# Kernel tuning notes

Hardware: AMD Instinct MI355X
Metric: run time of the kernel (lower is better)

Reference implementation:

```python
import jax, jax.numpy as jnp
import numpy as np

HEADS = 2


def _log_cpb(h, w, w1, b1, w2):
    # Swin-v2 style continuous relative position bias on an h*w grid.
    yy, xx = jnp.meshgrid(jnp.arange(h), jnp.arange(w), indexing='ij')
    coords = jnp.stack([yy.reshape(-1), xx.reshape(-1)], axis=-1).astype(jnp.float32)  # (L, 2)
    rel = coords[:, None, :] - coords[None, :, :]                                      # (L, L, 2)
    denom = jnp.array([max(h - 1, 1), max(w - 1, 1)], dtype=jnp.float32)
    rel = rel / denom * 8.0
    rel = jnp.sign(rel) * jnp.log2(1.0 + jnp.abs(rel)) / np.float32(np.log2(8.0))
    bias = jax.nn.relu(rel @ w1.T + b1) @ w2.T                                         # (L, L, heads)
    return jnp.transpose(bias, (2, 0, 1))                                              # (heads, L, L)


def setup_inputs() -> dict:
    key = jax.random.key(0)
    ks = jax.random.split(key, 11)
    b, s, c, h, w = 2, 32, 128, 24, 24
    hid, out_ch = 256, 128
    sc = lambda n: 1.0 / np.sqrt(n)
    return {
        'x':      jax.random.normal(ks[0], (b, s, c, h, w), jnp.float32),
        'qk_w':   jax.random.normal(ks[1], (2 * c, c), jnp.float32) * sc(c),
        'v_w':    jax.random.normal(ks[2], (hid, c), jnp.float32) * sc(c),
        'cpb_w1': jax.random.normal(ks[3], (c, 2), jnp.float32) * sc(2),
        'cpb_b1': jax.random.normal(ks[4], (c,), jnp.float32) * 0.02,
        'cpb_w2': jax.random.normal(ks[5], (HEADS, c), jnp.float32) * sc(c),
        'sa_bias': jax.random.uniform(ks[6], (hid, 1, 1), jnp.float32, -sc(c), sc(c)),
        'mlp_w1': jax.random.normal(ks[7], (hid, hid), jnp.float32) * sc(hid),
        'mlp_b1': jax.random.normal(ks[8], (hid,), jnp.float32) * 0.02,
        'mlp_w2': jax.random.normal(ks[9], (out_ch, hid), jnp.float32) * sc(hid),
        'mlp_b2': jax.random.normal(ks[10], (out_ch,), jnp.float32) * 0.02,
    }


def reference(x, qk_w, v_w, cpb_w1, cpb_b1, cpb_w2, sa_bias, mlp_w1, mlp_b1, mlp_w2, mlp_b2):
    b, s, c, h, w = x.shape
    L = h * w
    qkd = c // HEADS
    vd = v_w.shape[0] // HEADS
    xr = x.reshape(b * s, c, L)                                        # flatten (b s) and (h w)
    # QKV via 1x1 convs == channel matmuls
    qk = jnp.einsum('oc,bcl->bol', qk_w, xr)                           # (bs, 2c, L)
    qk = qk.reshape(b * s, 2, HEADS, qkd, L).transpose(1, 0, 2, 4, 3)  # (2, bs, heads, L, d)
    q, k = qk[0], qk[1]
    v = jnp.einsum('oc,bcl->bol', v_w, xr).reshape(b * s, HEADS, vd, L).transpose(0, 1, 3, 2)
    # learned continuous relative position bias, added as SDPA attn_mask
    bias = _log_cpb(h, w, cpb_w1, cpb_b1, cpb_w2)                      # (heads, L, L)
    scale = np.float32(1.0 / np.sqrt(qkd))
    scores = jnp.einsum('bhld,bhmd->bhlm', q, k) * scale + bias[None]
    attn = jax.nn.softmax(scores, axis=-1)
    out = jnp.einsum('bhlm,bhmd->bhld', attn, v)                       # (bs, heads, L, vd)
    out = out.transpose(0, 1, 3, 2).reshape(b, s, HEADS * vd, h, w)
    out = out + sa_bias[None, None]                                    # (b, s, hid, h, w)
    # 1x1-conv MLP with exact GELU
    y = jnp.einsum('oi,bsihw->bsohw', mlp_w1, out) + mlp_b1[None, None, :, None, None]
    y = jax.nn.gelu(y, approximate=False)
    y = jnp.einsum('oi,bsihw->bsohw', mlp_w2, y) + mlp_b2[None, None, :, None, None]
    return y
```

## Files before the change

### kernel.cpp

```cpp
#include <hip/hip_runtime.h>
#include <cstdint>
#include <cstddef>

constexpr int BS   = 64;
constexpr int Cc   = 128;
constexpr int Lc   = 576;
constexpr int VD   = 128;
constexpr int HID  = 256;
constexpr int OUTC = 128;
constexpr int NPIX = BS * Lc;

typedef __bf16 bf16x8 __attribute__((ext_vector_type(8)));
typedef float  f32x4  __attribute__((ext_vector_type(4)));
typedef unsigned short u16x8 __attribute__((ext_vector_type(8)));
typedef unsigned int   u32x4 __attribute__((ext_vector_type(4)));

__device__ __forceinline__ unsigned short f2bf(float f) {
  unsigned int u = __builtin_bit_cast(unsigned int, f);
  u += 0x7fffu + ((u >> 16) & 1u);
  return (unsigned short)(u >> 16);
}
__device__ __forceinline__ float bf2f(unsigned short h) {
  unsigned int u = ((unsigned int)h) << 16;
  return __builtin_bit_cast(float, u);
}
__device__ __forceinline__ unsigned int packhl(float v) {
  unsigned short hi = f2bf(v);
  unsigned short lo = f2bf(v - bf2f(hi));
  return ((unsigned int)hi << 16) | (unsigned int)lo;
}
__device__ __forceinline__ void unpack8(u32x4 a, u32x4 b, bf16x8& hi, bf16x8& lo) {
  u32x4 h, l;
  h[0] = (a[1] & 0xffff0000u) | (a[0] >> 16);
  l[0] = (a[1] << 16)         | (a[0] & 0xffffu);
  h[1] = (a[3] & 0xffff0000u) | (a[2] >> 16);
  l[1] = (a[3] << 16)         | (a[2] & 0xffffu);
  h[2] = (b[1] & 0xffff0000u) | (b[0] >> 16);
  l[2] = (b[1] << 16)         | (b[0] & 0xffffu);
  h[3] = (b[3] & 0xffff0000u) | (b[2] >> 16);
  l[3] = (b[3] << 16)         | (b[2] & 0xffffu);
  hi = __builtin_bit_cast(bf16x8, h);
  lo = __builtin_bit_cast(bf16x8, l);
}

#define MFMA16(a, b, c) __builtin_amdgcn_mfma_f32_16x16x32_bf16((a), (b), (c), 0, 0, 0)

__global__ __launch_bounds__(256) void cpb_kernel(const float* __restrict__ w1,
                                                  const float* __restrict__ b1,
                                                  const float* __restrict__ w2,
                                                  float* __restrict__ tab) {
  int idx = blockIdx.x * 256 + threadIdx.x;
  if (idx >= 47 * 47) return;
  int dy = idx / 47 - 23, dx = idx % 47 - 23;
  float fy = (float)dy * (8.0f / 23.0f);
  float fx = (float)dx * (8.0f / 23.0f);
  fy = copysignf(log2f(1.0f + fabsf(fy)) * (1.0f / 3.0f), fy);
  fx = copysignf(log2f(1.0f + fabsf(fx)) * (1.0f / 3.0f), fx);
  float a0 = 0.f, a1 = 0.f;
  for (int hh = 0; hh < 128; hh++) {
    float hv = fmaxf(w1[2 * hh] * fy + w1[2 * hh + 1] * fx + b1[hh], 0.f);
    a0 += w2[hh] * hv;
    a1 += w2[128 + hh] * hv;
  }
  tab[idx] = a0;
  tab[2209 + idx] = a1;
}

__global__ __launch_bounds__(256) void bias_mat(const float* __restrict__ tab,
                                                unsigned short* __restrict__ biasC) {
  int id = blockIdx.x * 256 + threadIdx.x;
  if (id >= 737280) return;
  int id2 = id % 2560;
  int grp = id / 2560;
  int wave = grp & 3;
  int mt = (grp >> 2) % 36;
  int hh = grp / 144;
  int g = id2 / 512;
  int lane = (id2 >> 3) & 63;
  int k = id2 & 7;
  int e = g * 8 + k;
  unsigned short val = 0;
  if (e < 36) {
    int ln = e >> 2, r = e & 3;
    int nt = wave * 9 + ln;
    int i = mt * 16 + (lane >> 4) * 4 + r;
    int j = nt * 16 + (lane & 15);
    int yi = i / 24, xi = i - yi * 24;
    int yj = j / 24, xj = j - yj * 24;
    val = f2bf(tab[hh * 2209 + (yi - yj + 23) * 47 + (xi - xj + 23)]);
  }
  biasC[id] = val;
}

__global__ __launch_bounds__(256) void prep_w(
    const float* __restrict__ w1, const float* __restrict__ w2,
    const float* __restrict__ qkw, const float* __restrict__ vw,
    unsigned short* __restrict__ w1h, unsigned short* __restrict__ w1l,
    unsigned short* __restrict__ w2h, unsigned short* __restrict__ w2l,
    unsigned short* __restrict__ wqkh, unsigned short* __restrict__ wqkl,
    unsigned short* __restrict__ wvh, unsigned short* __restrict__ wvl) {
  int id = blockIdx.x * 256 + threadIdx.x;
  const float* src;
  unsigned short *dh, *dl;
  int off;
  if (id < 65536)       { src = w1;  dh = w1h;  dl = w1l;  off = id; }
  else if (id < 98304)  { src = w2;  dh = w2h;  dl = w2l;  off = id - 65536; }
  else if (id < 131072) { src = qkw; dh = wqkh; dl = wqkl; off = id - 98304; }
  else if (id < 163840) { src = vw;  dh = wvh;  dl = wvl;  off = id - 131072; }
  else return;
  float v = src[off];
  unsigned short hi = f2bf(v);
  dh[off] = hi;
  dl[off] = f2bf(v - bf2f(hi));
}

__global__ __launch_bounds__(256) void prep_x(const float* __restrict__ x,
                                              unsigned short* __restrict__ xph,
                                              unsigned short* __restrict__ xpl) {
  __shared__ float xt[128 * 65];
  const int l0 = blockIdx.x * 64, bs = blockIdx.y;
  const int t = threadIdx.x;
  const float* xb = x + (size_t)bs * Cc * Lc;
#pragma unroll
  for (int pass = 0; pass < 8; pass++) {
    int f = pass * 1024 + t * 4;
    int c = f >> 6, ll = f & 63;
    *(float4*)(xt + c * 65 + ll) = *(const float4*)(xb + c * Lc + l0 + ll);
  }
  __syncthreads();
  const int rowl = t >> 2, c0 = (t & 3) * 32;
  const size_t p = (size_t)bs * Lc + l0 + rowl;
  unsigned short hbuf[32], lbuf[32];
#pragma unroll
  for (int i = 0; i < 32; i++) {
    float v = xt[(c0 + i) * 65 + rowl];
    unsigned short hi = f2bf(v);
    hbuf[i] = hi;
    lbuf[i] = f2bf(v - bf2f(hi));
  }
#pragma unroll
  for (int g = 0; g < 4; g++) {
    *(u16x8*)(xph + p * 128 + c0 + g * 8) = *(u16x8*)(hbuf + g * 8);
    *(u16x8*)(xpl + p * 128 + c0 + g * 8) = *(u16x8*)(lbuf + g * 8);
  }
}

__global__ __launch_bounds__(256, 2) void qkv_mfma(
    const unsigned short* __restrict__ xh, const unsigned short* __restrict__ xl,
    const unsigned short* __restrict__ wqkh, const unsigned short* __restrict__ wqkl,
    const unsigned short* __restrict__ wvh, const unsigned short* __restrict__ wvl,
    unsigned short* __restrict__ qg, unsigned short* __restrict__ kg,
    unsigned short* __restrict__ vg) {
  __shared__ unsigned short vt[128 * 130];
  const int t = threadIdx.x;
  const int wv = t >> 6, lane = t & 63;
  const int quad = lane >> 4, cc = lane & 15;
  const int by = blockIdx.y;
  const int n0 = (wv >> 1) * 64;
  const unsigned short* Wh = (by < 2) ? wqkh : wvh;
  const unsigned short* Wl = (by < 2) ? wqkl : wvl;
  const int wrow0 = (by & 1) * 128 + n0;
  f32x4 acc[4][4];
#pragma unroll
  for (int i = 0; i < 4; i++)
#pragma unroll
    for (int j = 0; j < 4; j++) acc[i][j] = (f32x4){0.f, 0.f, 0.f, 0.f};
  {
    const int srow = lane >> 3;
    const int schunk = (lane & 7) ^ srow;
    const size_t grow = (size_t)(blockIdx.x * 128 + wv * 32 + srow) * 128;
    const unsigned short* asrc = (schunk < 4)
                                     ? (xh + grow + (schunk << 3))
                                     : (xl + grow + ((schunk - 4) << 3));
    unsigned short* adst = vt + wv * 2048;
#pragma unroll
    for (int s = 0; s < 4; s++)
      __builtin_amdgcn_global_load_lds(
          (const __attribute__((address_space(1))) unsigned int*)(asrc + s * 1024),
          (__attribute__((address_space(3))) unsigned int*)(adst + s * 512),
          16, 0, 0);
    for (int kc = 0; kc < 4; kc++) {
      __syncthreads();
      const int bufo = (kc & 1) << 13;
      bf16x8 Ah[4], Al[4], Bh[4], Bl[4];
#pragma unroll
      for (int i = 0; i < 4; i++) {
        const int row = (wv & 1) * 64 + i * 16 + cc;
        const unsigned short* ab = vt + bufo + row * 64;
        Ah[i] = *(const bf16x8*)(ab + ((quad ^ (cc & 7)) << 3));
        Al[i] = *(const bf16x8*)(ab + (((quad + 4) ^ (cc & 7)) << 3));
      }
      if (kc < 3) {
        const int nb = ((kc + 1) & 1) << 13;
#pragma unroll
        for (int s = 0; s < 4; s++)
          __builtin_amdgcn_global_load_lds(
              (const __attribute__((address_space(1))) unsigned int*)(
                  asrc + (kc + 1) * 32 + s * 1024),
              (__attribute__((address_space(3))) unsigned int*)(adst + nb +
                                                                s * 512),
              16, 0, 0);
      }
      const int kb = kc * 32 + quad * 8;
#pragma unroll
      for (int i = 0; i < 4; i++) {
        size_t br = (size_t)(wrow0 + i * 16 + cc) * 128 + kb;
        Bh[i] = *(const bf16x8*)(Wh + br);
        Bl[i] = *(const bf16x8*)(Wl + br);
      }
#pragma unroll
      for (int i = 0; i < 4; i++)
#pragma unroll
        for (int j = 0; j < 4; j++) {
          acc[i][j] = MFMA16(Ah[i], Bh[j], acc[i][j]);
          acc[i][j] = MFMA16(Al[i], Bh[j], acc[i][j]);
          acc[i][j] = MFMA16(Ah[i], Bl[j], acc[i][j]);
        }
    }
  }
  __syncthreads();
  if (by < 2) {
    const float sc = (by == 0) ? 0.125f : 1.0f;
#pragma unroll
    for (int j = 0; j < 4; j++) {
      int o = n0 + j * 16 + cc;
#pragma unroll
      for (int i = 0; i < 4; i++)
#pragma unroll
        for (int r = 0; r < 4; r++) {
          int pl = (wv & 1) * 64 + i * 16 + quad * 4 + r;
          vt[pl * 130 + o] = f2bf(acc[i][j][r] * sc);
        }
    }
    __syncthreads();
    unsigned short* dst = (by == 0) ? qg : kg;
    const int pl = t >> 1, head = t & 1;
    const int p = blockIdx.x * 128 + pl;
    const int bs = p / 576, l = p - bs * 576;
    unsigned short* drow = dst + ((size_t)(bs * 2 + head) * Lc + l) * 64;
#pragma unroll
    for (int g = 0; g < 8; g++)
      *(u16x8*)(drow + g * 8) = *(const u16x8*)(vt + pl * 130 + head * 64 + g * 8);
  } else {
    const int head = by - 2;
#pragma unroll
    for (int j = 0; j < 4; j++) {
      int d = n0 + j * 16 + cc;
#pragma unroll
      for (int i = 0; i < 4; i++)
#pragma unroll
        for (int r = 0; r < 4; r++) {
          int pl = (wv & 1) * 64 + i * 16 + quad * 4 + r;
          vt[d * 130 + pl] = f2bf(acc[i][j][r]);
        }
    }
    __syncthreads();
    const int d = t >> 1, half = (t & 1) * 64;
#pragma unroll
    for (int c8 = 0; c8 < 8; c8++) {
      int pl = half + c8 * 8;
      int p = blockIdx.x * 128 + pl;
      int bs = p / 576, l = p - bs * 576;
      *(u16x8*)(vg + ((size_t)(bs * 2 + head) * VD + d) * Lc + l) =
          *(u16x8*)(vt + d * 130 + pl);
    }
  }
}

__global__ __launch_bounds__(256, 4) void attn_kernel(
    const unsigned short* __restrict__ qg,
    const unsigned short* __restrict__ kg,
    const unsigned short* __restrict__ vg,
    const unsigned short* __restrict__ biasC,
    const float* __restrict__ sa_bias,
    unsigned int* __restrict__ aout_p) {
  constexpr int PP = 580;
  __shared__ unsigned short Pb[32 * PP];
  __shared__ float psum[4][32];
  const int pair = blockIdx.x;
  const int hh = pair & 1, bs = pair >> 1;
  const int bm = blockIdx.y;
  const int m0 = bm * 32;
  const int t = threadIdx.x;
  const int wv = t >> 6, lane = t & 63;
  const int quad = lane >> 4, c = lane & 15;
  const unsigned short* qb = qg + ((size_t)pair * Lc + m0) * 64;
  const unsigned short* kb = kg + (size_t)pair * Lc * 64;
  const unsigned short* vb = vg + (size_t)pair * VD * Lc;
  bf16x8 qa0[2], qa1[2];
#pragma unroll
  for (int mt = 0; mt < 2; mt++) {
    const unsigned short* qp = qb + (size_t)(mt * 16 + c) * 64 + quad * 8;
    qa0[mt] = *(const bf16x8*)qp;
    qa1[mt] = *(const bf16x8*)(qp + 32);
  }
  f32x4 S[2][9];
#pragma unroll
  for (int mt = 0; mt < 2; mt++) {
    const unsigned short* bbase =
        biasC + ((((size_t)hh * 36 + (bm * 2 + mt)) * 4 + wv) * 5) * 512;
#pragma unroll
    for (int g = 0; g < 5; g++) {
      u16x8 bv = *(const u16x8*)(bbase + g * 512 + lane * 8);
#pragma unroll
      for (int k = 0; k < 8; k++) {
        int e = g * 8 + k;
        if (e < 36) S[mt][e >> 2][e & 3] = bf2f(bv[k]);
      }
    }
  }
#pragma unroll
  for (int ln = 0; ln < 9; ln++) {
    int nt = wv * 9 + ln;
    const unsigned short* kp = kb + (size_t)(nt * 16 + c) * 64 + quad * 8;
    bf16x8 b0 = *(const bf16x8*)kp;
    bf16x8 b1 = *(const bf16x8*)(kp + 32);
#pragma unroll
    for (int mt = 0; mt < 2; mt++)
      S[mt][ln] = MFMA16(qa1[mt], b1, MFMA16(qa0[mt], b0, S[mt][ln]));
  }
  float sm[2][4] = {{0.f, 0.f, 0.f, 0.f}, {0.f, 0.f, 0.f, 0.f}};
#pragma unroll
  for (int mt = 0; mt < 2; mt++)
#pragma unroll
    for (int ln = 0; ln < 9; ln++)
#pragma unroll
      for (int r = 0; r < 4; r++) {
        float e = __expf(S[mt][ln][r]);
        sm[mt][r] += e;
        Pb[(mt * 16 + quad * 4 + r) * PP + (wv * 9 + ln) * 16 + c] = f2bf(e);
      }
#pragma unroll
  for (int sh = 1; sh < 16; sh <<= 1)
#pragma unroll
    for (int mt = 0; mt < 2; mt++)
#pragma unroll
      for (int r = 0; r < 4; r++) sm[mt][r] += __shfl_xor(sm[mt][r], sh);
  if (c == 0)
#pragma unroll
    for (int mt = 0; mt < 2; mt++)
#pragma unroll
      for (int r = 0; r < 4; r++)
        psum[wv][mt * 16 + quad * 4 + r] = sm[mt][r];
  __syncthreads();
  float inv[2][4];
#pragma unroll
  for (int mt = 0; mt < 2; mt++)
#pragma unroll
    for (int r = 0; r < 4; r++) {
      int row = mt * 16 + quad * 4 + r;
      inv[mt][r] =
          1.0f / (psum[0][row] + psum[1][row] + psum[2][row] + psum[3][row]);
    }
  const int nd0 = wv * 2;
  f32x4 O[2][2];
#pragma unroll
  for (int mt = 0; mt < 2; mt++)
#pragma unroll
    for (int dd = 0; dd < 2; dd++) O[mt][dd] = (f32x4){0.f, 0.f, 0.f, 0.f};
#pragma unroll
  for (int kc = 0; kc < 18; kc++) {
    bf16x8 pa[2];
#pragma unroll
    for (int mt = 0; mt < 2; mt++)
      pa[mt] = *(const bf16x8*)(Pb + (size_t)(mt * 16 + c) * PP + kc * 32 +
                                quad * 8);
#pragma unroll
    for (int dd = 0; dd < 2; dd++) {
      bf16x8 vf = *(const bf16x8*)(vb + (size_t)((nd0 + dd) * 16 + c) * Lc +
                                   kc * 32 + quad * 8);
#pragma unroll
      for (int mt = 0; mt < 2; mt++) O[mt][dd] = MFMA16(pa[mt], vf, O[mt][dd]);
    }
  }
  unsigned int* obp = aout_p + ((size_t)bs * Lc + m0) * HID + hh * 128;
#pragma unroll
  for (int dd = 0; dd < 2; dd++) {
    float sb = sa_bias[hh * 128 + (nd0 + dd) * 16 + c];
#pragma unroll
    for (int mt = 0; mt < 2; mt++)
#pragma unroll
      for (int r = 0; r < 4; r++) {
        float v = O[mt][dd][r] * inv[mt][r] + sb;
        obp[(size_t)(mt * 16 + quad * 4 + r) * HID + (nd0 + dd) * 16 + c] =
            packhl(v);
      }
  }
}

__global__ __launch_bounds__(256, 4) void mlp_fused(
    const unsigned int* __restrict__ ap,
    const unsigned short* __restrict__ w1h, const unsigned short* __restrict__ w1l,
    const float* __restrict__ b1,
    const unsigned short* __restrict__ w2h, const unsigned short* __restrict__ w2l,
    const float* __restrict__ b2, float* __restrict__ out) {
  constexpr int YPW = 260;
  __shared__ unsigned int lds[32 * YPW];
  const int t = threadIdx.x;
  const int wv = t >> 6, lane = t & 63;
  const int quad = lane >> 4, cc = lane & 15;
  const int c7 = cc & 7;
  const int M0 = blockIdx.x * 32;

  const unsigned int* gsrc = ap + (size_t)(M0 + 8 * wv + (lane >> 3)) * HID +
                             (((lane & 7) ^ (lane >> 3)) << 2);
  __builtin_amdgcn_global_load_lds(
      (const __attribute__((address_space(1))) unsigned int*)gsrc,
      (__attribute__((address_space(3))) unsigned int*)(&lds[wv * 256]),
      16, 0, 0);

  const int n0 = wv * 64;
  f32x4 acc1[2][4];
#pragma unroll
  for (int i = 0; i < 2; i++)
#pragma unroll
    for (int j = 0; j < 4; j++) acc1[i][j] = (f32x4){0.f, 0.f, 0.f, 0.f};
  for (int kc = 0; kc < 8; kc++) {
    __syncthreads();
    const int bufw = (kc & 1) << 10;
    bf16x8 Ah[2], Al[2];
#pragma unroll
    for (int i = 0; i < 2; i++) {
      const int row = i * 16 + cc;
      u32x4 pa = *(const u32x4*)&lds[bufw + row * 32 + (((2 * quad) ^ c7) << 2)];
      u32x4 pb =
          *(const u32x4*)&lds[bufw + row * 32 + (((2 * quad + 1) ^ c7) << 2)];
      unpack8(pa, pb, Ah[i], Al[i]);
    }
    if (kc < 7) {
      __builtin_amdgcn_global_load_lds(
          (const __attribute__((address_space(1))) unsigned int*)(gsrc +
                                                                  (kc + 1) * 32),
          (__attribute__((address_space(3))) unsigned int*)(
              &lds[(((kc + 1) & 1) << 10) + wv * 256]),
          16, 0, 0);
    }
    const int kb = kc * 32 + quad * 8;
    bf16x8 Bh[4], Bl[4];
#pragma unroll
    for (int j = 0; j < 4; j++) {
      size_t br = (size_t)(n0 + j * 16 + cc) * HID + kb;
      Bh[j] = *(const bf16x8*)(w1h + br);
      Bl[j] = *(const bf16x8*)(w1l + br);
    }
#pragma unroll
    for (int i = 0; i < 2; i++)
#pragma unroll
      for (int j = 0; j < 4; j++) {
        acc1[i][j] = MFMA16(Ah[i], Bh[j], acc1[i][j]);
        acc1[i][j] = MFMA16(Al[i], Bh[j], acc1[i][j]);
        acc1[i][j] = MFMA16(Ah[i], Bl[j], acc1[i][j]);
      }
  }
  __syncthreads();
#pragma unroll
  for (int j = 0; j < 4; j++) {
    int col = n0 + j * 16 + cc;
    float bias = b1[col];
#pragma unroll
    for (int i = 0; i < 2; i++)
#pragma unroll
      for (int r = 0; r < 4; r++) {
        int row = i * 16 + quad * 4 + r;
        float v = acc1[i][j][r] + bias;
        float g = 0.5f * v * (1.0f + erff(v * 0.70710678118654752f));
        lds[row * YPW + col] = packhl(g);
      }
  }
  __syncthreads();
  {
    const int n2 = wv * 32;
    f32x4 acc2[2][2];
#pragma unroll
    for (int i = 0; i < 2; i++)
#pragma unroll
      for (int j = 0; j < 2; j++) acc2[i][j] = (f32x4){0.f, 0.f, 0.f, 0.f};
    for (int kc = 0; kc < 8; kc++) {
      const int kb = kc * 32 + quad * 8;
      bf16x8 Ah[2], Al[2], Bh[2], Bl[2];
#pragma unroll
      for (int i = 0; i < 2; i++) {
        const unsigned int* arow = &lds[(i * 16 + cc) * YPW + kb];
        u32x4 pa = *(const u32x4*)arow;
        u32x4 pb = *(const u32x4*)(arow + 4);
        unpack8(pa, pb, Ah[i], Al[i]);
      }
#pragma unroll
      for (int j = 0; j < 2; j++) {
        size_t br = (size_t)(n2 + j * 16 + cc) * HID + kb;
        Bh[j] = *(const bf16x8*)(w2h + br);
        Bl[j] = *(const bf16x8*)(w2l + br);
      }
#pragma unroll
      for (int i = 0; i < 2; i++)
#pragma unroll
        for (int j = 0; j < 2; j++) {
          acc2[i][j] = MFMA16(Ah[i], Bh[j], acc2[i][j]);
          acc2[i][j] = MFMA16(Al[i], Bh[j], acc2[i][j]);
          acc2[i][j] = MFMA16(Ah[i], Bl[j], acc2[i][j]);
        }
    }
#pragma unroll
    for (int i = 0; i < 2; i++) {
      int p = M0 + i * 16 + quad * 4;
      int bs = p / Lc, l = p - bs * Lc;
#pragma unroll
      for (int j = 0; j < 2; j++) {
        int col = n2 + j * 16 + cc;
        float bias = b2[col];
        float4 v = make_float4(acc2[i][j][0] + bias, acc2[i][j][1] + bias,
                               acc2[i][j][2] + bias, acc2[i][j][3] + bias);
        *(float4*)(out + ((size_t)bs * OUTC + col) * Lc + l) = v;
      }
    }
  }
}

extern "C" void kernel_launch(void* const* d_in, const int* in_sizes, int n_in,
                              void* d_out, int out_size, void* d_ws, size_t ws_size,
                              hipStream_t stream) {
  const float* x    = (const float*)d_in[0];
  const float* qk_w = (const float*)d_in[1];
  const float* v_w  = (const float*)d_in[2];
  const float* cw1  = (const float*)d_in[3];
  const float* cb1  = (const float*)d_in[4];
  const float* cw2  = (const float*)d_in[5];
  const float* sab  = (const float*)d_in[6];
  const float* mw1  = (const float*)d_in[7];
  const float* mb1  = (const float*)d_in[8];
  const float* mw2  = (const float*)d_in[9];
  const float* mb2  = (const float*)d_in[10];
  float* out = (float*)d_out;
  char* ws = (char*)d_ws;

  float* tab = (float*)(ws);
  unsigned short* biasC  = (unsigned short*)(ws + 65536);
  unsigned short* qg     = (unsigned short*)(ws + 1572864);
  unsigned short* kg     = (unsigned short*)(ws + 11010048);
  unsigned short* vg     = (unsigned short*)(ws + 20447232);
  unsigned short* xph    = (unsigned short*)(ws + 39321600);
  unsigned short* xpl    = (unsigned short*)(ws + 48758784);
  unsigned int*   aout_p = (unsigned int*)(ws + 58195968);
  unsigned short* w1h    = (unsigned short*)(ws + 95944704);
  unsigned short* w1l    = (unsigned short*)(ws + 96075776);
  unsigned short* w2h    = (unsigned short*)(ws + 96206848);
  unsigned short* w2l    = (unsigned short*)(ws + 96272384);
  unsigned short* wqkh   = (unsigned short*)(ws + 96337920);
  unsigned short* wqkl   = (unsigned short*)(ws + 96403456);
  unsigned short* wvh    = (unsigned short*)(ws + 96468992);
  unsigned short* wvl    = (unsigned short*)(ws + 96534528);

  cpb_kernel<<<dim3(9), dim3(256), 0, stream>>>(cw1, cb1, cw2, tab);
  bias_mat<<<dim3(2880), dim3(256), 0, stream>>>(tab, biasC);
  prep_w<<<dim3(640), dim3(256), 0, stream>>>(mw1, mw2, qk_w, v_w,
                                              w1h, w1l, w2h, w2l,
                                              wqkh, wqkl, wvh, wvl);
  prep_x<<<dim3(9, 64), dim3(256), 0, stream>>>(x, xph, xpl);
  qkv_mfma<<<dim3(288, 4), dim3(256), 0, stream>>>(xph, xpl, wqkh, wqkl,
                                                   wvh, wvl, qg, kg, vg);
  attn_kernel<<<dim3(128, 18), dim3(256), 0, stream>>>(qg, kg, vg, biasC, sab,
                                                       aout_p);
  mlp_fused<<<dim3(1152), dim3(256), 0, stream>>>(aout_p, w1h, w1l, mb1,
                                                  w2h, w2l, mb2, out);
}
```

Measured before the change: 269.4 us.

## Stage K tiles through LDS with async triple-buffered loads and swizzled grid order

Changes the K-tile loads in the attention score phase from direct global vector loads into asynchronous global-to-LDS copies. They are triple-buffered with an XOR swizzle and explicit vmcnt waits, so fetches overlap the MFMA work. It also flattens the 2D grid into a 1D order that interleaves 8 (batch,head) pairs per group of row tiles, aiming at better L2 locality across concurrently running blocks. The K staging reuses the probability buffer's LDS and adds a block-wide barrier. The hand-written waitcnt sequencing adds correctness risk.

```diff
diff --git a/kernel.cpp b/kernel.cpp
--- a/kernel.cpp
+++ b/kernel.cpp
@@ -277,13 +277,16 @@
   constexpr int PP = 580;
   __shared__ unsigned short Pb[32 * PP];
   __shared__ float psum[4][32];
-  const int pair = blockIdx.x;
+  const int f = blockIdx.x;
+  const int g = f >> 3;
+  const int pair = (f & 7) + 8 * (g / 18);
+  const int bm = g % 18;
   const int hh = pair & 1, bs = pair >> 1;
-  const int bm = blockIdx.y;
   const int m0 = bm * 32;
   const int t = threadIdx.x;
   const int wv = t >> 6, lane = t & 63;
   const int quad = lane >> 4, c = lane & 15;
+  const int c7 = c & 7;
   const unsigned short* qb = qg + ((size_t)pair * Lc + m0) * 64;
   const unsigned short* kb = kg + (size_t)pair * Lc * 64;
   const unsigned short* vb = vg + (size_t)pair * VD * Lc;
@@ -300,25 +303,59 @@
     const unsigned short* bbase =
         biasC + ((((size_t)hh * 36 + (bm * 2 + mt)) * 4 + wv) * 5) * 512;
 #pragma unroll
-    for (int g = 0; g < 5; g++) {
-      u16x8 bv = *(const u16x8*)(bbase + g * 512 + lane * 8);
+    for (int g2 = 0; g2 < 5; g2++) {
+      u16x8 bv = *(const u16x8*)(bbase + g2 * 512 + lane * 8);
 #pragma unroll
       for (int k = 0; k < 8; k++) {
-        int e = g * 8 + k;
+        int e = g2 * 8 + k;
         if (e < 36) S[mt][e >> 2][e & 3] = bf2f(bv[k]);
       }
     }
   }
-#pragma unroll
-  for (int ln = 0; ln < 9; ln++) {
-    int nt = wv * 9 + ln;
-    const unsigned short* kp = kb + (size_t)(nt * 16 + c) * 64 + quad * 8;
-    bf16x8 b0 = *(const bf16x8*)kp;
-    bf16x8 b1 = *(const bf16x8*)(kp + 32);
-#pragma unroll
-    for (int mt = 0; mt < 2; mt++)
-      S[mt][ln] = MFMA16(qa1[mt], b1, MFMA16(qa0[mt], b0, S[mt][ln]));
-  }
+  {
+    unsigned short* Ks = Pb + wv * 1024;
+    const int srow = lane >> 3;
+    const unsigned short* ksrc = kb + (size_t)(wv * 144 + srow) * 64 +
+                                 (((lane & 7) ^ srow) << 3);
+#pragma unroll
+    for (int tt = 0; tt < 2; tt++)
+#pragma unroll
+      for (int s = 0; s < 2; s++)
+        __builtin_amdgcn_global_load_lds(
+            (const __attribute__((address_space(1))) unsigned int*)(
+                ksrc + tt * 1024 + s * 512),
+            (__attribute__((address_space(3))) unsigned int*)(
+                Ks + tt * 4096 + s * 512),
+            16, 0, 0);
+#pragma unroll
+    for (int ln = 0; ln < 9; ln++) {
+      if (ln + 2 < 9) {
+        asm volatile("s_waitcnt lgkmcnt(0)" ::: "memory");
+        __builtin_amdgcn_sched_barrier(0);
+#pragma unroll
+        for (int s = 0; s < 2; s++)
+          __builtin_amdgcn_global_load_lds(
+              (const __attribute__((address_space(1))) unsigned int*)(
+                  ksrc + (ln + 2) * 1024 + s * 512),
+              (__attribute__((address_space(3))) unsigned int*)(
+                  Ks + ((ln + 2) % 3) * 4096 + s * 512),
+              16, 0, 0);
+        asm volatile("s_waitcnt vmcnt(4)" ::: "memory");
+      } else if (ln == 7) {
+        asm volatile("s_waitcnt vmcnt(2)" ::: "memory");
+      } else {
+        asm volatile("s_waitcnt vmcnt(0)" ::: "memory");
+      }
+      __builtin_amdgcn_sched_barrier(0);
+      const unsigned short* kbuf = Ks + (ln % 3) * 4096;
+      bf16x8 b0 = *(const bf16x8*)(kbuf + c * 64 + ((quad ^ c7) << 3));
+      bf16x8 b1 = *(const bf16x8*)(kbuf + c * 64 + (((quad + 4) ^ c7) << 3));
+#pragma unroll
+      for (int mt = 0; mt < 2; mt++)
+        S[mt][ln] = MFMA16(qa1[mt], b1, MFMA16(qa0[mt], b0, S[mt][ln]));
+    }
+  }
+  __syncthreads();
   float sm[2][4] = {{0.f, 0.f, 0.f, 0.f}, {0.f, 0.f, 0.f, 0.f}};
 #pragma unroll
   for (int mt = 0; mt < 2; mt++)
@@ -558,8 +595,8 @@
   prep_x<<<dim3(9, 64), dim3(256), 0, stream>>>(x, xph, xpl);
   qkv_mfma<<<dim3(288, 4), dim3(256), 0, stream>>>(xph, xpl, wqkh, wqkl,
                                                    wvh, wvl, qg, kg, vg);
-  attn_kernel<<<dim3(128, 18), dim3(256), 0, stream>>>(qg, kg, vg, biasC, sab,
-                                                       aout_p);
+  attn_kernel<<<dim3(2304), dim3(256), 0, stream>>>(qg, kg, vg, biasC, sab,
+                                                    aout_p);
   mlp_fused<<<dim3(1152), dim3(256), 0, stream>>>(aout_p, w1h, w1l, mb1,
                                                   w2h, w2l, mb2, out);
 }
```

Result: faster. 260.2 us (-3.4%).
